# Performance work log

Hardware: AMD Instinct MI355X
Metric: run time of the kernel (lower is better)

## Reference

```python
import jax, jax.numpy as jnp
import numpy as np

D_MODEL = 512
N_HEADS = 8
D_KV = 64
INNER = N_HEADS * D_KV
NUM_BUCKETS = 32
MAX_DISTANCE = 128
LN_EPS = 1e-6


def _relative_position_bucket(rel, num_buckets=NUM_BUCKETS, max_distance=MAX_DISTANCE):
    # bidirectional T5 bucketing
    nb = num_buckets // 2
    buckets = (rel > 0).astype(jnp.int32) * nb
    rel = jnp.abs(rel)
    max_exact = nb // 2
    is_small = rel < max_exact
    relf = jnp.maximum(rel.astype(jnp.float32), 1.0)  # guard log(0)
    large = max_exact + (
        jnp.log(relf / max_exact) / np.log(max_distance / max_exact) * (nb - max_exact)
    ).astype(jnp.int32)
    large = jnp.minimum(large, nb - 1)
    return buckets + jnp.where(is_small, rel, large)


def t5_layer_norm(x, weight, eps=LN_EPS):
    # T5 LayerNorm: no mean subtraction, no bias
    var = jnp.mean(jnp.square(x), axis=-1, keepdims=True)
    return x * jax.lax.rsqrt(var + eps) * weight


def compute_position_bias(rel_bias_table, q_len, k_len):
    ctx = jnp.arange(q_len)[:, None]
    mem = jnp.arange(k_len)[None, :]
    buckets = _relative_position_bucket(mem - ctx)  # [q, k]
    bias = rel_bias_table[buckets]                  # [q, k, H]
    return jnp.transpose(bias, (2, 0, 1))[None]     # [1, H, q, k]


def setup_inputs() -> dict:
    key = jax.random.key(0)
    ks = jax.random.split(key, 8)
    N, S = 8, 2048
    s = 1.0 / np.sqrt(D_MODEL)
    return {
        "hidden_states": jax.random.normal(ks[0], (N, S, D_MODEL), jnp.float32),
        "ln_weight": jnp.ones((D_MODEL,), jnp.float32),
        "wq": jax.random.normal(ks[1], (D_MODEL, INNER), jnp.float32) * s,
        "wk": jax.random.normal(ks[2], (D_MODEL, INNER), jnp.float32) * s,
        "wv": jax.random.normal(ks[3], (D_MODEL, INNER), jnp.float32) * s,
        "wo": jax.random.normal(ks[4], (INNER, D_MODEL), jnp.float32) * s,
        "rel_bias_table": jax.random.normal(ks[5], (NUM_BUCKETS, N_HEADS), jnp.float32) * 0.1,
        "seq_idx2graph_idx": jax.random.randint(ks[6], (8,), 0, 8, jnp.int64) if jax.config.jax_enable_x64 else jax.random.randint(ks[6], (8,), 0, 8, jnp.int32),
    }


def reference(hidden_states, ln_weight, wq, wk, wv, wo, rel_bias_table, seq_idx2graph_idx):
    N, S, _ = hidden_states.shape
    normed = t5_layer_norm(hidden_states, ln_weight)

    # T5Attention (no 1/sqrt(d) scaling in T5)
    q = jnp.einsum("nsd,de->nse", normed, wq).reshape(N, S, N_HEADS, D_KV)
    k = jnp.einsum("nsd,de->nse", normed, wk).reshape(N, S, N_HEADS, D_KV)
    v = jnp.einsum("nsd,de->nse", normed, wv).reshape(N, S, N_HEADS, D_KV)

    position_bias = compute_position_bias(rel_bias_table, S, S)  # [1,H,S,S]
    scores = jnp.einsum("nqhd,nkhd->nhqk", q, k) + position_bias
    attn = jax.nn.softmax(scores, axis=-1)
    ctx = jnp.einsum("nhqk,nkhd->nqhd", attn, v).reshape(N, S, INNER)
    attn_out = jnp.einsum("nse,ed->nsd", ctx, wo)

    # residual (dropout is identity in eval)
    hidden = hidden_states + attn_out
    remain_node_idx = jnp.arange(seq_idx2graph_idx.shape[0])
    return hidden, position_bias, remain_node_idx
```

## Files before the change

kernel.cpp:

```cpp
#include <hip/hip_runtime.h>
#include <hip/hip_bf16.h>
#include <math.h>

typedef __bf16 bf16;
typedef bf16 bf16x8 __attribute__((ext_vector_type(8)));
typedef bf16 bf16x4 __attribute__((ext_vector_type(4)));
typedef float f32x4 __attribute__((ext_vector_type(4)));
typedef float f32x16 __attribute__((ext_vector_type(16)));

#define MFMA16(a, b, c) __builtin_amdgcn_mfma_f32_16x16x32_bf16(a, b, c, 0, 0, 0)
#define MFMA32(a, b, c) __builtin_amdgcn_mfma_f32_32x32x16_bf16(a, b, c, 0, 0, 0)
#define LOG2E 1.4426950408889634f
#define NEG_SHIFT -40.0f

__device__ __forceinline__ void glds16(const bf16* g, bf16* l) {
  __builtin_amdgcn_global_load_lds(
      (const __attribute__((address_space(1))) void*)g,
      (__attribute__((address_space(3))) void*)l, 16, 0, 0);
}

__device__ inline unsigned pkbf(float a, float b) {
  union { bf16 h; unsigned short u; } ca, cb;
  ca.h = (bf16)a;
  cb.h = (bf16)b;
  return (unsigned)ca.u | ((unsigned)cb.u << 16);
}

__device__ inline float t5bias(const float* __restrict__ table, int h, int x) {
  if (x > 4094) return 0.f;
  int rel = x - 2047;
  int bucket = (rel > 0) ? 16 : 0;
  int ar = rel < 0 ? -rel : rel;
  int v;
  if (ar < 8) {
    v = ar;
  } else {
    double tt = log((double)ar / 8.0) / log(16.0) * 8.0;
    int lg = 8 + (int)tt;
    v = lg < 15 ? lg : 15;
  }
  return table[(bucket + v) * 8 + h];
}

__global__ __launch_bounds__(256) void prep_kernel(
    const float* __restrict__ hidden, const float* __restrict__ ln_w,
    const float* __restrict__ wq, const float* __restrict__ wk,
    const float* __restrict__ wv, const float* __restrict__ wo,
    const float* __restrict__ table, bf16* __restrict__ normed,
    float* __restrict__ lut, float4* __restrict__ lutq,
    float* __restrict__ out_remain, bf16* __restrict__ wt_qkv,
    bf16* __restrict__ wt_o) {
  __shared__ float tile[32][33];
  int bid = blockIdx.x;
  int t = threadIdx.x;
  if (bid < 4096) {
    int row = bid * 4 + (t >> 6);
    int lane = t & 63;
    const float4* xr = (const float4*)(hidden + (size_t)row * 512);
    float4 a = xr[lane];
    float4 b = xr[lane + 64];
    float s = a.x * a.x + a.y * a.y + a.z * a.z + a.w * a.w +
              b.x * b.x + b.y * b.y + b.z * b.z + b.w * b.w;
#pragma unroll
    for (int off = 32; off > 0; off >>= 1) s += __shfl_down(s, off, 64);
    float tot = __shfl(s, 0, 64);
    float rscale = rsqrtf(tot * (1.0f / 512.0f) + 1e-6f);
    float4 w0 = *(const float4*)(ln_w + 4 * lane);
    float4 w1 = *(const float4*)(ln_w + 256 + 4 * lane);
    bf16x4 o0, o1;
    o0[0] = (bf16)(a.x * rscale * w0.x);
    o0[1] = (bf16)(a.y * rscale * w0.y);
    o0[2] = (bf16)(a.z * rscale * w0.z);
    o0[3] = (bf16)(a.w * rscale * w0.w);
    o1[0] = (bf16)(b.x * rscale * w1.x);
    o1[1] = (bf16)(b.y * rscale * w1.y);
    o1[2] = (bf16)(b.z * rscale * w1.z);
    o1[3] = (bf16)(b.w * rscale * w1.w);
    *(bf16x4*)(normed + (size_t)row * 512 + 4 * lane) = o0;
    *(bf16x4*)(normed + (size_t)row * 512 + 256 + 4 * lane) = o1;
  } else if (bid < 4224) {
    int i = (bid - 4096) * 256 + t;
    int h = i >> 12;
    int d = i & 4095;
    lut[(size_t)h * 4096 + d] = t5bias(table, h, d);
    if (i < 8) out_remain[i] = (float)i;
  } else if (bid < 5248) {
    int bid2 = bid - 4224;
    int mat = bid2 >> 8;
    int rem = bid2 & 255;
    int e0 = (rem & 15) * 32;
    int k0 = (rem >> 4) * 32;
    int tx = t & 31, ty = t >> 5;
    const float* W = (mat == 0) ? wq : (mat == 1) ? wk : (mat == 2) ? wv : wo;
#pragma unroll
    for (int j = 0; j < 32; j += 8)
      tile[ty + j][tx] = W[(size_t)(k0 + ty + j) * 512 + e0 + tx];
    __syncthreads();
    bf16* dst = (mat < 3) ? (wt_qkv + (size_t)mat * 512 * 512) : wt_o;
#pragma unroll
    for (int j = 0; j < 32; j += 8)
      dst[(size_t)(e0 + ty + j) * 512 + k0 + tx] = (bf16)tile[tx][ty + j];
  } else {
    int i = (bid - 5248) * 256 + t;
    int h = i >> 12;
    int d = i & 4095;
    float4 o;
    o.x = t5bias(table, h, d);
    o.y = t5bias(table, h, d + 1);
    o.z = t5bias(table, h, d + 2);
    o.w = t5bias(table, h, d + 3);
    lutq[(size_t)h * 4096 + d] = o;
  }
}

__global__ __launch_bounds__(256) void qkv_gemm(
    const bf16* __restrict__ normed, const bf16* __restrict__ wt,
    bf16* __restrict__ qb, bf16* __restrict__ kb, bf16* __restrict__ vtb) {
  __shared__ __align__(16) char smem[19456];
  bf16* As = (bf16*)smem;
  bf16* Bs = (bf16*)(smem + 8192);
  int t = threadIdx.x;
  int wave = t >> 6, lane = t & 63;
  int quad = lane >> 4, lc = lane & 15;
  int wm = wave >> 1, wn = wave & 1;
  int m0 = blockIdx.x * 128, n0 = blockIdx.y * 128;

  f32x4 acc[4][4];
#pragma unroll
  for (int i = 0; i < 4; i++)
#pragma unroll
    for (int j = 0; j < 4; j++) acc[i][j] = (f32x4){0.f, 0.f, 0.f, 0.f};

  int rw = lane >> 2;
  int c8 = (lane & 3) * 8;
  const bf16* gA = normed + (size_t)(m0 + wave * 32 + rw) * 512 + c8;
  const bf16* gB = wt + (size_t)(n0 + wave * 32 + rw) * 512 + c8;
  bf16* lA = As + wave * 1024;
  bf16* lB = Bs + wave * 1024;

  for (int kt = 0; kt < 16; ++kt) {
    int k0 = kt * 32;
    __syncthreads();
    glds16(gA + k0, lA);
    glds16(gA + 16 * 512 + k0, lA + 512);
    glds16(gB + k0, lB);
    glds16(gB + 16 * 512 + k0, lB + 512);
    __syncthreads();
    bf16x8 af[4], bfr[4];
#pragma unroll
    for (int i = 0; i < 4; i++)
      af[i] = *(const bf16x8*)&As[(wm * 64 + i * 16 + lc) * 32 + quad * 8];
#pragma unroll
    for (int j = 0; j < 4; j++)
      bfr[j] = *(const bf16x8*)&Bs[(wn * 64 + j * 16 + lc) * 32 + quad * 8];
#pragma unroll
    for (int i = 0; i < 4; i++)
#pragma unroll
      for (int j = 0; j < 4; j++)
        acc[i][j] = MFMA16(af[i], bfr[j], acc[i][j]);
  }

  __syncthreads();
  int mat = n0 >> 9;
  int e_base = (n0 & 511) + wn * 64;
  int hh = e_base >> 6;
  int grow0 = m0 + wm * 64;
  int nbi = grow0 >> 11, sbase = grow0 & 2047;

  if (mat == 2) {
    bf16* dv = vtb + ((size_t)(nbi * 8 + hh) * 64) * 2048;
#pragma unroll
    for (int i = 0; i < 4; i++) {
      int s = sbase + i * 16 + quad * 4;
#pragma unroll
      for (int j = 0; j < 4; j++) {
        int d = j * 16 + lc;
        bf16x4 o4;
#pragma unroll
        for (int r = 0; r < 4; r++) o4[r] = (bf16)acc[i][j][r];
        *(bf16x4*)(dv + (size_t)d * 2048 + s) = o4;
      }
    }
  } else {
    bf16* dst0 = (mat == 0) ? qb : kb;
    bf16* dst = dst0 + (((size_t)nbi * 8 + hh) * 2048 + sbase) * 64;
    bf16* Cw = (bf16*)smem + wave * 2432;
#pragma unroll
    for (int p = 0; p < 2; ++p) {
#pragma unroll
      for (int i2 = 0; i2 < 2; ++i2) {
#pragma unroll
        for (int j = 0; j < 4; ++j)
#pragma unroll
          for (int r = 0; r < 4; ++r)
            Cw[(i2 * 16 + quad * 4 + r) * 76 + j * 16 + lc] =
                (bf16)acc[2 * p + i2][j][r];
      }
#pragma unroll
      for (int c = 0; c < 4; ++c) {
        bf16x8 vch =
            *(const bf16x8*)&Cw[(c * 8 + (lane >> 3)) * 76 + (lane & 7) * 8];
        *(bf16x8*)(dst + (size_t)(p * 32 + c * 8 + (lane >> 3)) * 64 +
                   (lane & 7) * 8) = vch;
      }
    }
  }
}

__global__ __launch_bounds__(256, 3) void attn_bias_kernel(
    const bf16* __restrict__ qg, const bf16* __restrict__ kg,
    const bf16* __restrict__ vtg, const float4* __restrict__ lutq,
    const float* __restrict__ lutg, bf16* __restrict__ ctx,
    float* __restrict__ bias_out) {
  __shared__ bf16 Ks[64][72];
  __shared__ bf16 Vs[64][72];
  int t = threadIdx.x;

  if (blockIdx.x >= 1024) {
    size_t i = (((size_t)blockIdx.x - 1024) * 256 + t) * 4;
    int h = (int)(i >> 22);
    int q = (int)((i >> 11) & 2047);
    int k = (int)(i & 2047);
    const float* lh = lutg + (size_t)h * 4096 + (2047 - q);
    float4 v = {lh[k], lh[k + 1], lh[k + 2], lh[k + 3]};
    *(float4*)(bias_out + i) = v;
    return;
  }

  int id = blockIdx.x;
  int xcd = id & 7, slot = id >> 3;
  int bh = xcd * 8 + (slot >> 4);
  int qt = slot & 15;
  int n = bh >> 3, h = bh & 7;
  int q0 = qt * 128;

  int wave = t >> 6, lane = t & 63;
  int l31 = lane & 31, hi = lane >> 5;
  int q = q0 + wave * 32 + l31;

  const float4* bq = lutq + (size_t)h * 4096;
  int cbase = 2047 + 4 * hi - q;

  const bf16* qp = qg + ((size_t)bh * 2048 + q) * 64;
  bf16x8 Qf[4];
#pragma unroll
  for (int c = 0; c < 4; c++) Qf[c] = *(const bf16x8*)(qp + c * 16 + hi * 8);

  f32x16 O[2];
#pragma unroll
  for (int i = 0; i < 2; i++)
#pragma unroll
    for (int e = 0; e < 16; e++) O[i][e] = 0.f;
  float lsum0 = 0.f, lsum1 = 0.f;

  int srow = t >> 2, scol = (t & 3) * 16;
  const bf16* kp = kg + (size_t)bh * 2048 * 64;
  const bf16* vp = vtg + (size_t)bh * 64 * 2048;

  bf16x8 kv0 = *(const bf16x8*)(kp + (size_t)srow * 64 + scol);
  bf16x8 kv1 = *(const bf16x8*)(kp + (size_t)srow * 64 + scol + 8);
  bf16x8 vv0 = *(const bf16x8*)(vp + (size_t)srow * 2048 + scol);
  bf16x8 vv1 = *(const bf16x8*)(vp + (size_t)srow * 2048 + scol + 8);

  for (int kt = 0; kt < 32; ++kt) {
    int kr0 = kt * 64;
    __syncthreads();
    *(bf16x8*)&Ks[srow][scol] = kv0;
    *(bf16x8*)&Ks[srow][scol + 8] = kv1;
    *(bf16x8*)&Vs[srow][scol] = vv0;
    *(bf16x8*)&Vs[srow][scol + 8] = vv1;
    __syncthreads();

    f32x16 st[2];
#pragma unroll
    for (int mi = 0; mi < 2; mi++)
#pragma unroll
      for (int g = 0; g < 4; g++) {
        float4 b4 = bq[cbase + kr0 + mi * 32 + 8 * g];
        st[mi][4 * g + 0] = b4.x;
        st[mi][4 * g + 1] = b4.y;
        st[mi][4 * g + 2] = b4.z;
        st[mi][4 * g + 3] = b4.w;
      }

    if (kt + 1 < 32) {
      int kn = kr0 + 64;
      kv0 = *(const bf16x8*)(kp + (size_t)(kn + srow) * 64 + scol);
      kv1 = *(const bf16x8*)(kp + (size_t)(kn + srow) * 64 + scol + 8);
      vv0 = *(const bf16x8*)(vp + (size_t)srow * 2048 + kn + scol);
      vv1 = *(const bf16x8*)(vp + (size_t)srow * 2048 + kn + scol + 8);
    }

#pragma unroll
    for (int mi = 0; mi < 2; mi++) {
#pragma unroll
      for (int c = 0; c < 4; c++) {
        bf16x8 kf = *(const bf16x8*)&Ks[mi * 32 + l31][c * 16 + hi * 8];
        st[mi] = MFMA32(kf, Qf[c], st[mi]);
      }
      unsigned D[8], X[8];
#pragma unroll
      for (int g = 0; g < 4; g++) {
#pragma unroll
        for (int e = 0; e < 4; e++) {
          float p = __builtin_amdgcn_exp2f(fmaf(st[mi][4 * g + e], LOG2E, NEG_SHIFT));
          st[mi][4 * g + e] = p;
          if (e & 1) lsum1 += p; else lsum0 += p;
        }
        D[2 * g] = pkbf(st[mi][4 * g + 0], st[mi][4 * g + 1]);
        D[2 * g + 1] = pkbf(st[mi][4 * g + 2], st[mi][4 * g + 3]);
      }
#pragma unroll
      for (int tt = 0; tt < 8; tt++) X[tt] = __shfl_xor(D[tt], 32, 64);

#pragma unroll
      for (int kk = 0; kk < 2; kk++) {
        int kc = 2 * mi + kk;
        int b = 4 * kk;
        unsigned f0 = hi ? X[b + 2] : D[b + 0];
        unsigned f1 = hi ? X[b + 3] : D[b + 1];
        unsigned f2 = hi ? D[b + 2] : X[b + 0];
        unsigned f3 = hi ? D[b + 3] : X[b + 1];
        union { uint4 u; bf16x8 v; } cv;
        cv.u = make_uint4(f0, f1, f2, f3);
        bf16x8 pf = cv.v;
#pragma unroll
        for (int md = 0; md < 2; md++) {
          bf16x8 vf = *(const bf16x8*)&Vs[md * 32 + l31][kc * 16 + hi * 8];
          O[md] = MFMA32(vf, pf, O[md]);
        }
      }
    }
  }

  float l_run = lsum0 + lsum1;
  l_run += __shfl_xor(l_run, 32, 64);
  float inv = 1.0f / l_run;
  bf16* cp = ctx + ((size_t)n * 2048 + q) * 512 + h * 64;
#pragma unroll
  for (int md = 0; md < 2; md++)
#pragma unroll
    for (int g = 0; g < 4; g++) {
      bf16x4 o4;
#pragma unroll
      for (int e = 0; e < 4; e++) o4[e] = (bf16)(O[md][4 * g + e] * inv);
      *(bf16x4*)(cp + md * 32 + 8 * g + hi * 4) = o4;
    }
}

__global__ __launch_bounds__(256) void oproj_gemm(
    const bf16* __restrict__ ctx, const bf16* __restrict__ wt_o,
    const float* __restrict__ hidden, float* __restrict__ out) {
  __shared__ __align__(16) char smem[16384];
  bf16* As = (bf16*)smem;
  bf16* Bs = (bf16*)(smem + 8192);
  int t = threadIdx.x;
  int wave = t >> 6, lane = t & 63;
  int quad = lane >> 4, lc = lane & 15;
  int wm = wave >> 1, wn = wave & 1;
  int m0 = blockIdx.x * 128, n0 = blockIdx.y * 128;

  f32x4 acc[4][4];
#pragma unroll
  for (int i = 0; i < 4; i++)
#pragma unroll
    for (int j = 0; j < 4; j++) acc[i][j] = (f32x4){0.f, 0.f, 0.f, 0.f};

  int rw = lane >> 2;
  int c8 = (lane & 3) * 8;
  const bf16* gA = ctx + (size_t)(m0 + wave * 32 + rw) * 512 + c8;
  const bf16* gB = wt_o + (size_t)(n0 + wave * 32 + rw) * 512 + c8;
  bf16* lA = As + wave * 1024;
  bf16* lB = Bs + wave * 1024;

  for (int kt = 0; kt < 16; ++kt) {
    int k0 = kt * 32;
    __syncthreads();
    glds16(gA + k0, lA);
    glds16(gA + 16 * 512 + k0, lA + 512);
    glds16(gB + k0, lB);
    glds16(gB + 16 * 512 + k0, lB + 512);
    __syncthreads();
    bf16x8 af[4], bfr[4];
#pragma unroll
    for (int i = 0; i < 4; i++)
      af[i] = *(const bf16x8*)&As[(wm * 64 + i * 16 + lc) * 32 + quad * 8];
#pragma unroll
    for (int j = 0; j < 4; j++)
      bfr[j] = *(const bf16x8*)&Bs[(wn * 64 + j * 16 + lc) * 32 + quad * 8];
#pragma unroll
    for (int i = 0; i < 4; i++)
#pragma unroll
      for (int j = 0; j < 4; j++)
        acc[i][j] = MFMA16(af[i], bfr[j], acc[i][j]);
  }

#pragma unroll
  for (int i = 0; i < 4; i++) {
#pragma unroll
    for (int j = 0; j < 4; j++) {
#pragma unroll
      for (int r = 0; r < 4; r++) {
        int grow = m0 + wm * 64 + i * 16 + quad * 4 + r;
        int gcol = n0 + wn * 64 + j * 16 + lc;
        size_t idx = (size_t)grow * 512 + gcol;
        out[idx] = acc[i][j][r] + hidden[idx];
      }
    }
  }
}

extern "C" void kernel_launch(void* const* d_in, const int* in_sizes, int n_in,
                              void* d_out, int out_size, void* d_ws, size_t ws_size,
                              hipStream_t stream) {
  const float* hidden = (const float*)d_in[0];
  const float* ln_w = (const float*)d_in[1];
  const float* wq = (const float*)d_in[2];
  const float* wk = (const float*)d_in[3];
  const float* wv = (const float*)d_in[4];
  const float* wo = (const float*)d_in[5];
  const float* table = (const float*)d_in[6];

  float* out_hidden = (float*)d_out;
  float* out_bias = out_hidden + (size_t)8 * 2048 * 512;
  float* out_remain = out_bias + (size_t)8 * 2048 * 2048;

  char* ws = (char*)d_ws;
  bf16* normed = (bf16*)(ws + 0);
  float* lut = (float*)(ws + 16777216);
  float4* lutq = (float4*)(ws + 16908288);
  bf16* wt_qkv = (bf16*)(ws + 17432576);
  bf16* wt_o = (bf16*)(ws + 19005440);
  bf16* qb = (bf16*)(ws + 19529728);
  bf16* kb = qb + (size_t)8 * 8 * 2048 * 64;
  bf16* vtb = kb + (size_t)8 * 8 * 2048 * 64;
  bf16* ctx = normed;

  prep_kernel<<<dim3(5376), dim3(256), 0, stream>>>(
      hidden, ln_w, wq, wk, wv, wo, table, normed, lut, lutq, out_remain,
      wt_qkv, wt_o);
  qkv_gemm<<<dim3(128, 12), dim3(256), 0, stream>>>(normed, wt_qkv, qb, kb, vtb);
  attn_bias_kernel<<<dim3(1024 + 32768), dim3(256), 0, stream>>>(
      qb, kb, vtb, lutq, lut, ctx, out_bias);
  oproj_gemm<<<dim3(128, 4), dim3(256), 0, stream>>>(ctx, wt_o, hidden, out_hidden);
}
```

Baseline: 360.7 us.

## Double-buffer attention K/V tiles, fold softmax scaling into Q and bias LUT, move bias write

The attention kernel now double-buffers K/V tiles in LDS, leaving one barrier per tile instead of two, and prefetches the next tile's bias values right after the exp. The log2(e) scale and the constant shift are moved into the Q projection output and the bias LUT, which removes an FMA per score. The cross-half data exchange uses v_permlane32_swap instead of shuffles, and MFMA sections get raised wave priority. The 64 MB position-bias write moves from the attention launch into the output-projection launch, with four float4 stores per thread. Scaling Q by log2(e) before the bf16 cast changes rounding slightly, and occupancy is raised to 4 blocks per CU.

```diff
diff --git a/kernel.cpp b/kernel.cpp
--- a/kernel.cpp
+++ b/kernel.cpp
@@ -5,6 +5,7 @@
 typedef __bf16 bf16;
 typedef bf16 bf16x8 __attribute__((ext_vector_type(8)));
 typedef bf16 bf16x4 __attribute__((ext_vector_type(4)));
+typedef float f32x2 __attribute__((ext_vector_type(2)));
 typedef float f32x4 __attribute__((ext_vector_type(4)));
 typedef float f32x16 __attribute__((ext_vector_type(16)));
 
@@ -24,6 +25,10 @@
   ca.h = (bf16)a;
   cb.h = (bf16)b;
   return (unsigned)ca.u | ((unsigned)cb.u << 16);
+}
+
+__device__ __forceinline__ void pl32swap(unsigned& a, unsigned& b) {
+  asm("v_permlane32_swap_b32 %0, %1" : "+v"(a), "+v"(b));
 }
 
 __device__ inline float t5bias(const float* __restrict__ table, int h, int x) {
@@ -105,10 +110,10 @@
     int h = i >> 12;
     int d = i & 4095;
     float4 o;
-    o.x = t5bias(table, h, d);
-    o.y = t5bias(table, h, d + 1);
-    o.z = t5bias(table, h, d + 2);
-    o.w = t5bias(table, h, d + 3);
+    o.x = t5bias(table, h, d) * LOG2E + NEG_SHIFT;
+    o.y = t5bias(table, h, d + 1) * LOG2E + NEG_SHIFT;
+    o.z = t5bias(table, h, d + 2) * LOG2E + NEG_SHIFT;
+    o.w = t5bias(table, h, d + 3) * LOG2E + NEG_SHIFT;
     lutq[(size_t)h * 4096 + d] = o;
   }
 }
@@ -182,6 +187,7 @@
       }
     }
   } else {
+    float qsc = (mat == 0) ? LOG2E : 1.0f;
     bf16* dst0 = (mat == 0) ? qb : kb;
     bf16* dst = dst0 + (((size_t)nbi * 8 + hh) * 2048 + sbase) * 64;
     bf16* Cw = (bf16*)smem + wave * 2432;
@@ -194,7 +200,7 @@
 #pragma unroll
           for (int r = 0; r < 4; ++r)
             Cw[(i2 * 16 + quad * 4 + r) * 76 + j * 16 + lc] =
-                (bf16)acc[2 * p + i2][j][r];
+                (bf16)(acc[2 * p + i2][j][r] * qsc);
       }
 #pragma unroll
       for (int c = 0; c < 4; ++c) {
@@ -207,25 +213,83 @@
   }
 }
 
-__global__ __launch_bounds__(256, 3) void attn_bias_kernel(
+#define LDB4(SV, G, V4)       \
+  {                           \
+    float4 _b = (V4);         \
+    SV[4 * (G) + 0] = _b.x;   \
+    SV[4 * (G) + 1] = _b.y;   \
+    SV[4 * (G) + 2] = _b.z;   \
+    SV[4 * (G) + 3] = _b.w;   \
+  }
+
+#define BODY(RB, WB, PF)                                                     \
+  {                                                                          \
+    if (PF) {                                                                \
+      kv0 = *(const bf16x8*)(kpc);                                           \
+      kv1 = *(const bf16x8*)(kpc + 8);                                       \
+      vv0 = *(const bf16x8*)(vpc);                                           \
+      vv1 = *(const bf16x8*)(vpc + 8);                                       \
+    }                                                                        \
+    _Pragma("unroll") for (int mi = 0; mi < 2; mi++) {                       \
+      __builtin_amdgcn_s_setprio(1);                                         \
+      _Pragma("unroll") for (int c = 0; c < 4; c++) {                        \
+        bf16x8 kf = *(const bf16x8*)&Ks[RB][mi * 32 + l31][c * 16 + hi * 8]; \
+        st[mi] = MFMA32(kf, Qf[c], st[mi]);                                  \
+      }                                                                      \
+      __builtin_amdgcn_s_setprio(0);                                         \
+      unsigned D[8];                                                         \
+      _Pragma("unroll") for (int g = 0; g < 4; g++) {                        \
+        _Pragma("unroll") for (int e = 0; e < 4; e++)                        \
+            st[mi][4 * g + e] = __builtin_amdgcn_exp2f(st[mi][4 * g + e]);   \
+        lsA += (f32x2){st[mi][4 * g + 0], st[mi][4 * g + 1]};                \
+        lsB += (f32x2){st[mi][4 * g + 2], st[mi][4 * g + 3]};                \
+        D[2 * g] = pkbf(st[mi][4 * g + 0], st[mi][4 * g + 1]);               \
+        D[2 * g + 1] = pkbf(st[mi][4 * g + 2], st[mi][4 * g + 3]);           \
+      }                                                                      \
+      if (PF) {         \
+        LDB4(st[mi], 0, bpn[mi * 32 + 0]);                                   \
+        LDB4(st[mi], 1, bpn[mi * 32 + 8]);                                   \
+        LDB4(st[mi], 2, bpn[mi * 32 + 16]);                                  \
+        LDB4(st[mi], 3, bpn[mi * 32 + 24]);                                  \
+      }                                                                      \
+      pl32swap(D[0], D[2]);                                                  \
+      pl32swap(D[1], D[3]);                                                  \
+      pl32swap(D[4], D[6]);                                                  \
+      pl32swap(D[5], D[7]);                                                  \
+      _Pragma("unroll") for (int kk = 0; kk < 2; kk++) {                     \
+        int kc = 2 * mi + kk;                                                \
+        union { uint4 u; bf16x8 v; } cv;                                     \
+        cv.u = make_uint4(D[4 * kk + 0], D[4 * kk + 1], D[4 * kk + 2],       \
+                          D[4 * kk + 3]);                                    \
+        bf16x8 pf = cv.v;                                                    \
+        __builtin_amdgcn_s_setprio(1);                                       \
+        _Pragma("unroll") for (int md = 0; md < 2; md++) {                   \
+          bf16x8 vf =                                                        \
+              *(const bf16x8*)&Vs[RB][md * 32 + l31][kc * 16 + hi * 8];      \
+          O[md] = MFMA32(vf, pf, O[md]);                                     \
+        }                                                                    \
+        __builtin_amdgcn_s_setprio(0);                                       \
+      }                                                                      \
+    }                                                                        \
+    if (PF) {                                                                \
+      *(bf16x8*)&Ks[WB][srow][scol] = kv0;                                   \
+      *(bf16x8*)&Ks[WB][srow][scol + 8] = kv1;                               \
+      *(bf16x8*)&Vs[WB][srow][scol] = vv0;                                   \
+      *(bf16x8*)&Vs[WB][srow][scol + 8] = vv1;                               \
+      kpc += 4096;                                                           \
+      vpc += 64;                                                             \
+      bpn += 64;                                                             \
+    }                                                                        \
+    __syncthreads();                                                         \
+  }
+
+__global__ __launch_bounds__(256, 4) void attn_kernel(
     const bf16* __restrict__ qg, const bf16* __restrict__ kg,
     const bf16* __restrict__ vtg, const float4* __restrict__ lutq,
-    const float* __restrict__ lutg, bf16* __restrict__ ctx,
-    float* __restrict__ bias_out) {
-  __shared__ bf16 Ks[64][72];
-  __shared__ bf16 Vs[64][72];
+    bf16* __restrict__ ctx) {
+  __shared__ bf16 Ks[2][64][72];
+  __shared__ bf16 Vs[2][64][72];
   int t = threadIdx.x;
-
-  if (blockIdx.x >= 1024) {
-    size_t i = (((size_t)blockIdx.x - 1024) * 256 + t) * 4;
-    int h = (int)(i >> 22);
-    int q = (int)((i >> 11) & 2047);
-    int k = (int)(i & 2047);
-    const float* lh = lutg + (size_t)h * 4096 + (2047 - q);
-    float4 v = {lh[k], lh[k + 1], lh[k + 2], lh[k + 3]};
-    *(float4*)(bias_out + i) = v;
-    return;
-  }
 
   int id = blockIdx.x;
   int xcd = id & 7, slot = id >> 3;
@@ -238,8 +302,7 @@
   int l31 = lane & 31, hi = lane >> 5;
   int q = q0 + wave * 32 + l31;
 
-  const float4* bq = lutq + (size_t)h * 4096;
-  int cbase = 2047 + 4 * hi - q;
+  const float4* bp = lutq + (size_t)h * 4096 + (2047 + 4 * hi - q);
 
   const bf16* qp = qg + ((size_t)bh * 2048 + q) * 64;
   bf16x8 Qf[4];
@@ -251,89 +314,43 @@
   for (int i = 0; i < 2; i++)
 #pragma unroll
     for (int e = 0; e < 16; e++) O[i][e] = 0.f;
-  float lsum0 = 0.f, lsum1 = 0.f;
+  f32x2 lsA = {0.f, 0.f}, lsB = {0.f, 0.f};
 
   int srow = t >> 2, scol = (t & 3) * 16;
-  const bf16* kp = kg + (size_t)bh * 2048 * 64;
-  const bf16* vp = vtg + (size_t)bh * 64 * 2048;
-
-  bf16x8 kv0 = *(const bf16x8*)(kp + (size_t)srow * 64 + scol);
-  bf16x8 kv1 = *(const bf16x8*)(kp + (size_t)srow * 64 + scol + 8);
-  bf16x8 vv0 = *(const bf16x8*)(vp + (size_t)srow * 2048 + scol);
-  bf16x8 vv1 = *(const bf16x8*)(vp + (size_t)srow * 2048 + scol + 8);
-
-  for (int kt = 0; kt < 32; ++kt) {
-    int kr0 = kt * 64;
-    __syncthreads();
-    *(bf16x8*)&Ks[srow][scol] = kv0;
-    *(bf16x8*)&Ks[srow][scol + 8] = kv1;
-    *(bf16x8*)&Vs[srow][scol] = vv0;
-    *(bf16x8*)&Vs[srow][scol + 8] = vv1;
-    __syncthreads();
-
-    f32x16 st[2];
-#pragma unroll
-    for (int mi = 0; mi < 2; mi++)
-#pragma unroll
-      for (int g = 0; g < 4; g++) {
-        float4 b4 = bq[cbase + kr0 + mi * 32 + 8 * g];
-        st[mi][4 * g + 0] = b4.x;
-        st[mi][4 * g + 1] = b4.y;
-        st[mi][4 * g + 2] = b4.z;
-        st[mi][4 * g + 3] = b4.w;
-      }
-
-    if (kt + 1 < 32) {
-      int kn = kr0 + 64;
-      kv0 = *(const bf16x8*)(kp + (size_t)(kn + srow) * 64 + scol);
-      kv1 = *(const bf16x8*)(kp + (size_t)(kn + srow) * 64 + scol + 8);
-      vv0 = *(const bf16x8*)(vp + (size_t)srow * 2048 + kn + scol);
-      vv1 = *(const bf16x8*)(vp + (size_t)srow * 2048 + kn + scol + 8);
-    }
-
-#pragma unroll
-    for (int mi = 0; mi < 2; mi++) {
-#pragma unroll
-      for (int c = 0; c < 4; c++) {
-        bf16x8 kf = *(const bf16x8*)&Ks[mi * 32 + l31][c * 16 + hi * 8];
-        st[mi] = MFMA32(kf, Qf[c], st[mi]);
-      }
-      unsigned D[8], X[8];
-#pragma unroll
-      for (int g = 0; g < 4; g++) {
-#pragma unroll
-        for (int e = 0; e < 4; e++) {
-          float p = __builtin_amdgcn_exp2f(fmaf(st[mi][4 * g + e], LOG2E, NEG_SHIFT));
-          st[mi][4 * g + e] = p;
-          if (e & 1) lsum1 += p; else lsum0 += p;
-        }
-        D[2 * g] = pkbf(st[mi][4 * g + 0], st[mi][4 * g + 1]);
-        D[2 * g + 1] = pkbf(st[mi][4 * g + 2], st[mi][4 * g + 3]);
-      }
-#pragma unroll
-      for (int tt = 0; tt < 8; tt++) X[tt] = __shfl_xor(D[tt], 32, 64);
-
-#pragma unroll
-      for (int kk = 0; kk < 2; kk++) {
-        int kc = 2 * mi + kk;
-        int b = 4 * kk;
-        unsigned f0 = hi ? X[b + 2] : D[b + 0];
-        unsigned f1 = hi ? X[b + 3] : D[b + 1];
-        unsigned f2 = hi ? D[b + 2] : X[b + 0];
-        unsigned f3 = hi ? D[b + 3] : X[b + 1];
-        union { uint4 u; bf16x8 v; } cv;
-        cv.u = make_uint4(f0, f1, f2, f3);
-        bf16x8 pf = cv.v;
-#pragma unroll
-        for (int md = 0; md < 2; md++) {
-          bf16x8 vf = *(const bf16x8*)&Vs[md * 32 + l31][kc * 16 + hi * 8];
-          O[md] = MFMA32(vf, pf, O[md]);
-        }
-      }
-    }
-  }
-
-  float l_run = lsum0 + lsum1;
+  const bf16* kp = kg + (size_t)bh * 2048 * 64 + srow * 64 + scol;
+  const bf16* vp = vtg + (size_t)bh * 64 * 2048 + (size_t)srow * 2048 + scol;
+
+  bf16x8 kv0 = *(const bf16x8*)(kp);
+  bf16x8 kv1 = *(const bf16x8*)(kp + 8);
+  bf16x8 vv0 = *(const bf16x8*)(vp);
+  bf16x8 vv1 = *(const bf16x8*)(vp + 8);
+  *(bf16x8*)&Ks[0][srow][scol] = kv0;
+  *(bf16x8*)&Ks[0][srow][scol + 8] = kv1;
+  *(bf16x8*)&Vs[0][srow][scol] = vv0;
+  *(bf16x8*)&Vs[0][srow][scol + 8] = vv1;
+  f32x16 st[2];
+  LDB4(st[0], 0, bp[0]);
+  LDB4(st[0], 1, bp[8]);
+  LDB4(st[0], 2, bp[16]);
+  LDB4(st[0], 3, bp[24]);
+  LDB4(st[1], 0, bp[32]);
+  LDB4(st[1], 1, bp[40]);
+  LDB4(st[1], 2, bp[48]);
+  LDB4(st[1], 3, bp[56]);
+  const bf16* kpc = kp + 4096;
+  const bf16* vpc = vp + 64;
+  const float4* bpn = bp + 64;
+  __syncthreads();
+
+#pragma unroll 1
+  for (int it = 0; it < 15; ++it) {
+    BODY(0, 1, 1)
+    BODY(1, 0, 1)
+  }
+  BODY(0, 1, 1)
+  BODY(1, 0, 0)
+
+  float l_run = lsA.x + lsA.y + lsB.x + lsB.y;
   l_run += __shfl_xor(l_run, 32, 64);
   float inv = 1.0f / l_run;
   bf16* cp = ctx + ((size_t)n * 2048 + q) * 512 + h * 64;
@@ -350,15 +367,33 @@
 
 __global__ __launch_bounds__(256) void oproj_gemm(
     const bf16* __restrict__ ctx, const bf16* __restrict__ wt_o,
-    const float* __restrict__ hidden, float* __restrict__ out) {
+    const float* __restrict__ hidden, float* __restrict__ out,
+    const float* __restrict__ lut, float* __restrict__ bias_out) {
   __shared__ __align__(16) char smem[16384];
+  int t = threadIdx.x;
+  int bid = blockIdx.x;
+
+  if (bid >= 512) {
+    int bb = bid - 512;
+#pragma unroll
+    for (int j = 0; j < 4; ++j) {
+      size_t i = ((size_t)bb * 1024 + j * 256 + t) * 4;
+      int h = (int)(i >> 22);
+      int q = (int)((i >> 11) & 2047);
+      int k = (int)(i & 2047);
+      const float* lh = lut + (size_t)h * 4096 + (2047 - q);
+      float4 v = {lh[k], lh[k + 1], lh[k + 2], lh[k + 3]};
+      *(float4*)(bias_out + i) = v;
+    }
+    return;
+  }
+
   bf16* As = (bf16*)smem;
   bf16* Bs = (bf16*)(smem + 8192);
-  int t = threadIdx.x;
   int wave = t >> 6, lane = t & 63;
   int quad = lane >> 4, lc = lane & 15;
   int wm = wave >> 1, wn = wave & 1;
-  int m0 = blockIdx.x * 128, n0 = blockIdx.y * 128;
+  int m0 = (bid & 127) * 128, n0 = (bid >> 7) * 128;
 
   f32x4 acc[4][4];
 #pragma unroll
@@ -440,7 +475,8 @@
       hidden, ln_w, wq, wk, wv, wo, table, normed, lut, lutq, out_remain,
       wt_qkv, wt_o);
   qkv_gemm<<<dim3(128, 12), dim3(256), 0, stream>>>(normed, wt_qkv, qb, kb, vtb);
-  attn_bias_kernel<<<dim3(1024 + 32768), dim3(256), 0, stream>>>(
-      qb, kb, vtb, lutq, lut, ctx, out_bias);
-  oproj_gemm<<<dim3(128, 4), dim3(256), 0, stream>>>(ctx, wt_o, hidden, out_hidden);
-}
+  attn_kernel<<<dim3(1024), dim3(256), 0, stream>>>(qb, kb, vtb, lutq, ctx);
+  oproj_gemm<<<dim3(512 + 8192), dim3(256), 0, stream>>>(ctx, wt_o, hidden,
+                                                         out_hidden, lut,
+                                                         out_bias);
+}
```

Result: slower. 380.4 us (+5.4%).
